# Kernel tuning notes

Hardware: AMD Instinct MI355X
Metric: run time of the kernel (lower is better)

The kernel has to match this reference:

```python
import jax, jax.numpy as jnp
import numpy as np

DECAY = 0.99
EPS = 1e-05


def setup_inputs() -> dict:
    key = jax.random.key(0)
    k1, k2 = jax.random.split(key)
    B, C, H, W = 16, 64, 32, 32
    K = 8192
    z_e = jax.random.normal(k1, (B, C, H, W), dtype=jnp.float32)
    embedding = jax.random.normal(k2, (K, C), dtype=jnp.float32)
    cluster_size = jnp.zeros((K,), dtype=jnp.float32)
    embedding_avg = embedding  # initialized as a clone of the codebook
    return {"z_e": z_e, "embedding": embedding, "cluster_size": cluster_size,
            "embedding_avg": embedding_avg}


def reference(z_e, embedding, cluster_size, embedding_avg):
    B, C, H, W = z_e.shape
    K = embedding.shape[0]
    # [N, C] tokens
    z_flat = jnp.transpose(z_e, (0, 2, 3, 1)).reshape(-1, C)
    d = ((z_flat * z_flat).sum(-1, keepdims=True)
         - 2.0 * (z_flat @ embedding.T)
         + (embedding * embedding).sum(-1))
    indices = jnp.argmin(d, axis=1)  # [N] int
    z_q_flat = embedding[indices]    # [N, C]
    z_q = jnp.transpose(z_q_flat.reshape(B, H, W, C), (0, 3, 1, 2))
    # EMA codebook update (training path); one-hot matmuls expressed as segment sums
    counts = jax.ops.segment_sum(jnp.ones(z_flat.shape[0], dtype=z_flat.dtype),
                                 indices, num_segments=K)            # encodings.sum(0)
    dw = jax.ops.segment_sum(z_flat, indices, num_segments=K)        # encodings.T @ z_flat
    new_cluster_size = DECAY * cluster_size + (1.0 - DECAY) * counts
    new_embedding_avg = DECAY * embedding_avg + (1.0 - DECAY) * dw
    n = new_cluster_size.sum()
    cs = (new_cluster_size + EPS) / (n + K * EPS) * n
    new_embedding = new_embedding_avg / cs[:, None]
    # straight-through estimator
    z_q_st = z_e + jax.lax.stop_gradient(z_q - z_e)
    return (z_q_st, indices.reshape(B, H * W), z_q,
            new_embedding, new_cluster_size, new_embedding_avg)
```

## Files before the change

kernel.cpp:

```cpp
#include <hip/hip_runtime.h>

#define DECAYF 0.99f
#define OMDF   0.01f
#define TAU    3.5e-2f

typedef unsigned int u32;
typedef unsigned long long u64;
typedef __attribute__((ext_vector_type(8))) _Float16 f16x8;
typedef __attribute__((ext_vector_type(16))) float f32x16;

#define EN_OFF     0
#define EFRAG_OFF  32768
#define IDX_OFF    32768
#define LIST_OFF   98304
#define BEST1_OFF  2129920
#define BEST2_OFF  3178496
#define CNT_OFF    3702784

__device__ __forceinline__ u64 enc_pair(float s, int idx) {
  u32 u = __float_as_uint(s);
  u = (u & 0x80000000u) ? ~u : (u | 0x80000000u);
  return ((u64)u << 32) | (u32)(~idx);
}
__device__ __forceinline__ float dec_score(u64 e) {
  u32 u = (u32)(e >> 32);
  u = (u & 0x80000000u) ? (u & 0x7fffffffu) : ~u;
  return __uint_as_float(u);
}
__device__ __forceinline__ int dec_idx(u64 e) { return (int)(~(u32)e); }
__device__ __forceinline__ unsigned short f2h(float f) {
  union { _Float16 h; unsigned short u; } v;
  v.h = (_Float16)f;
  return v.u;
}
__device__ __forceinline__ float exact_dot(const float* __restrict__ sx,
                                           const float* __restrict__ emb, int k) {
  const float4* e = (const float4*)(emb + (size_t)k * 64);
  float a = 0.f;
#pragma unroll
  for (int q = 0; q < 16; ++q) {
    float4 v = e[q];
    a = fmaf(sx[4 * q],     v.x, a);
    a = fmaf(sx[4 * q + 1], v.y, a);
    a = fmaf(sx[4 * q + 2], v.z, a);
    a = fmaf(sx[4 * q + 3], v.w, a);
  }
  return a;
}

__global__ __launch_bounds__(256) void k_prep(const float* __restrict__ emb,
                                              const float* __restrict__ cs_in,
                                              const float* __restrict__ avg_in,
                                              const float* __restrict__ z_e,
                                              float* __restrict__ en,
                                              unsigned char* __restrict__ efrag,
                                              unsigned char* __restrict__ zfrag,
                                              float* __restrict__ out4,
                                              float* __restrict__ out5,
                                              int* __restrict__ cnt,
                                              float* __restrict__ nsum) {
  __shared__ float warr[4];
  int bid = blockIdx.x;
  if (bid < 512) {
    int tid = bid * 256 + threadIdx.x;
    if (tid == 0) *cnt = 0;
    int k = tid >> 4, q = tid & 15;
    float4 v = ((const float4*)emb)[tid];
    int kstep = q >> 2, h = (q >> 1) & 1, j0 = (q & 1) * 4;
    int tile = k >> 5, n32 = k & 31;
    ushort4 hv;
    hv.x = f2h(v.x); hv.y = f2h(v.y); hv.z = f2h(v.z); hv.w = f2h(v.w);
    size_t off = (size_t)tile * 4096 + (size_t)kstep * 1024
               + (size_t)h * 512 + (size_t)n32 * 16 + (size_t)j0 * 2;
    *(ushort4*)(efrag + off) = hv;
    float s = v.x * v.x + v.y * v.y + v.z * v.z + v.w * v.w;
    s += __shfl_xor(s, 1, 16);
    s += __shfl_xor(s, 2, 16);
    s += __shfl_xor(s, 4, 16);
    s += __shfl_xor(s, 8, 16);
    if (q == 0) en[k] = 0.5f * s;
  } else if (bid < 1031) {
    int tid = (bid - 512) * 256 + threadIdx.x;
    if (tid < 131072) {
      float4 v = ((const float4*)avg_in)[tid];
      v.x *= DECAYF; v.y *= DECAYF; v.z *= DECAYF; v.w *= DECAYF;
      ((float4*)out5)[tid] = v;
    }
  } else if (bid == 1031) {
    int thr = threadIdx.x;
    float s = 0.f;
#pragma unroll
    for (int q = 0; q < 8; ++q) {
      int idx = q * 256 + thr;
      float4 v = ((const float4*)cs_in)[idx];
      v.x *= DECAYF; v.y *= DECAYF; v.z *= DECAYF; v.w *= DECAYF;
      ((float4*)out4)[idx] = v;
      s += v.x + v.y + v.z + v.w;
    }
    s += __shfl_xor(s, 1, 64);
    s += __shfl_xor(s, 2, 64);
    s += __shfl_xor(s, 4, 64);
    s += __shfl_xor(s, 8, 64);
    s += __shfl_xor(s, 16, 64);
    s += __shfl_xor(s, 32, 64);
    if ((thr & 63) == 0) warr[thr >> 6] = s;
    __syncthreads();
    if (thr == 0) *nsum = warr[0] + warr[1] + warr[2] + warr[3];
  } else {
    int t = (bid - 1032) * 256 + threadIdx.x;
    int m = t & 31, h = (t >> 5) & 1, ks = (t >> 6) & 3, tg = t >> 8;
    int token = tg * 32 + m;
    int b = token >> 10, hw = token & 1023;
    const float* zr = z_e + ((size_t)b << 16) + hw;
    int c0 = ks * 16 + h * 8;
    unsigned short u[8];
#pragma unroll
    for (int j = 0; j < 8; ++j) u[j] = f2h(zr[(size_t)(c0 + j) << 10]);
    size_t off = (size_t)tg * 4096 + (size_t)ks * 1024
               + (size_t)h * 512 + (size_t)m * 16;
    ((ushort4*)(zfrag + off))[0] = make_ushort4(u[0], u[1], u[2], u[3]);
    ((ushort4*)(zfrag + off))[1] = make_ushort4(u[4], u[5], u[6], u[7]);
  }
}

__global__ __launch_bounds__(256) void k_argmin_mfma(
    const unsigned char* __restrict__ zfrag,
    const unsigned char* __restrict__ efrag,
    const float* __restrict__ en, u64* __restrict__ best1,
    float* __restrict__ best2) {
  alignas(16) __shared__ unsigned char sbuf[2][8192];
  __shared__ float sen[1024];
  const int tb = blockIdx.x >> 3;
  const int sl = blockIdx.x & 7;
  const int wave = threadIdx.x >> 6, lane = threadIdx.x & 63;
  const int h = lane >> 5, m = lane & 31;
  const int token0 = tb * 128 + wave * 32;
  const int scb = sl << 10;

  ((float4*)sen)[threadIdx.x] = ((const float4*)(en + scb))[threadIdx.x];

  f16x8 a[4];
  {
    const unsigned char* zb = zfrag + ((size_t)(tb * 4 + wave)) * 4096
                            + (size_t)h * 512 + (size_t)m * 16;
#pragma unroll
    for (int ks = 0; ks < 4; ++ks) a[ks] = *(const f16x8*)(zb + (size_t)ks * 1024);
  }
  float b1[16], b2[16];
#pragma unroll
  for (int r = 0; r < 16; ++r) { b1[r] = -3.0e38f; b2[r] = -3.0e38f; }

  const unsigned char* gbase0 = efrag + (size_t)scb * 128;
  auto stage = [&](int ib, int buf) {
    const unsigned char* g = gbase0 + (size_t)ib * 8192 + (size_t)wave * 2048;
#pragma unroll
    for (int it = 0; it < 2; ++it) {
      __builtin_amdgcn_global_load_lds(
          (const __attribute__((address_space(1))) u32*)(g + it * 1024 + lane * 16),
          (__attribute__((address_space(3))) u32*)(&sbuf[buf][wave * 2048 + it * 1024]),
          16, 0, 0);
    }
  };
  stage(0, 0);
  for (int ib = 0; ib < 16; ++ib) {
    __syncthreads();
    if (ib < 15) stage(ib + 1, (ib + 1) & 1);
    const unsigned char* sb0 = &sbuf[ib & 1][0];
#pragma unroll
    for (int t32 = 0; t32 < 2; ++t32) {
      const int t = ib * 2 + t32;
      const float negen = -sen[t * 32 + m];
      f32x16 acc;
#pragma unroll
      for (int r = 0; r < 16; ++r) acc[r] = negen;
      const unsigned char* sb = sb0 + t32 * 4096 + h * 512 + m * 16;
#pragma unroll
      for (int ks = 0; ks < 4; ++ks) {
        f16x8 bf = *(const f16x8*)(sb + (size_t)ks * 1024);
        acc = __builtin_amdgcn_mfma_f32_32x32x16_f16(a[ks], bf, acc, 0, 0, 0);
      }
      const u32 emb6 = (u32)(63 - t);
#pragma unroll
      for (int r = 0; r < 16; ++r) {
        float f = __uint_as_float((__float_as_uint(acc[r]) & 0xFFFFFFC0u) | emb6);
        b2[r] = __builtin_amdgcn_fmed3f(f, b1[r], b2[r]);
        b1[r] = fmaxf(b1[r], f);
      }
    }
  }
  int mi[16];
#pragma unroll
  for (int r = 0; r < 16; ++r) mi[r] = m;
#pragma unroll
  for (int st = 1; st < 32; st <<= 1) {
#pragma unroll
    for (int r = 0; r < 16; ++r) {
      float ob1 = __shfl_xor(b1[r], st, 64);
      float ob2 = __shfl_xor(b2[r], st, 64);
      int omi = __shfl_xor(mi[r], st, 64);
      bool ogt = ob1 > b1[r];
      b2[r] = fmaxf(fminf(b1[r], ob1), fmaxf(b2[r], ob2));
      mi[r] = ogt ? omi : mi[r];
      b1[r] = fmaxf(b1[r], ob1);
    }
  }
  if (m == 0) {
#pragma unroll
    for (int r = 0; r < 16; ++r) {
      int row = (r & 3) + 8 * (r >> 2) + 4 * h;
      int token = token0 + row;
      int t = 63 - (int)(__float_as_uint(b1[r]) & 63u);
      int gcode = scb + t * 32 + mi[r];
      best1[(size_t)sl * 16384 + token] = enc_pair(b1[r], gcode);
      best2[(size_t)sl * 16384 + token] = b2[r];
    }
  }
}

__global__ __launch_bounds__(256) void k_resolve(const u64* __restrict__ best1,
                                                 const float* __restrict__ best2,
                                                 int* __restrict__ idxa,
                                                 int* __restrict__ list,
                                                 int* __restrict__ cnt) {
  int n = blockIdx.x * 256 + threadIdx.x;
  u64 e[8];
  float sp[8];
#pragma unroll
  for (int s = 0; s < 8; ++s) {
    e[s]  = best1[(size_t)s * 16384 + n];
    sp[s] = best2[(size_t)s * 16384 + n];
  }
  u64 top = e[0];
#pragma unroll
  for (int s = 1; s < 8; ++s) top = e[s] > top ? e[s] : top;
  float second = -3.0e38f;
#pragma unroll
  for (int s = 0; s < 8; ++s) second = fmaxf(second, sp[s]);
#pragma unroll
  for (int s = 0; s < 8; ++s)
    if (e[s] != top) second = fmaxf(second, dec_score(e[s]));
  idxa[n] = dec_idx(top);
  if (dec_score(top) - second < TAU) {
    int p = atomicAdd(cnt, 1);
    list[p] = n;
  }
}

__global__ __launch_bounds__(256) void k_fixup(const float* __restrict__ z_e,
                                               const float* __restrict__ emb,
                                               const float* __restrict__ en,
                                               const u64* __restrict__ best1,
                                               const float* __restrict__ best2,
                                               const int* __restrict__ list,
                                               const int* __restrict__ cnt,
                                               int* __restrict__ idxa) {
  __shared__ float sx[64];
  __shared__ u64 esh[8];
  __shared__ float b2sh[8];
  __shared__ int cand[8];
  __shared__ int fsl[8];
  __shared__ int ncand, nfsl;
  __shared__ u64 red;
  int count = *cnt;
  for (int i = blockIdx.x; i < count; i += gridDim.x) {
    int n = list[i];
    __syncthreads();
    if (threadIdx.x == 0) { ncand = 0; nfsl = 0; red = 0ull; }
    if (threadIdx.x < 8) {
      esh[threadIdx.x]  = best1[(size_t)threadIdx.x * 16384 + n];
      b2sh[threadIdx.x] = best2[(size_t)threadIdx.x * 16384 + n];
    }
    if (threadIdx.x < 64) {
      sx[threadIdx.x] = z_e[((size_t)(n >> 10) << 16)
                            + ((size_t)threadIdx.x << 10) + (n & 1023)];
    }
    __syncthreads();
    u64 top = esh[0];
#pragma unroll
    for (int s = 1; s < 8; ++s) top = esh[s] > top ? esh[s] : top;
    float theta = dec_score(top) - TAU;
    if (threadIdx.x < 8) {
      int s = threadIdx.x;
      if (dec_score(esh[s]) >= theta) {
        int p = atomicAdd(&ncand, 1);
        cand[p] = dec_idx(esh[s]);
      }
      if (b2sh[s] >= theta) {
        int p = atomicAdd(&nfsl, 1);
        fsl[p] = s;
      }
    }
    __syncthreads();
    u64 myb = 0ull;
    if (threadIdx.x < ncand) {
      int k = cand[threadIdx.x];
      float a = exact_dot(sx, emb, k) - en[k];
      myb = enc_pair(a, k);
    }
    int nf = nfsl;
    for (int f = 0; f < nf; ++f) {
      int s = fsl[f];
      int k0 = (s << 10) + threadIdx.x;
      float a0 = exact_dot(sx, emb, k0)       - en[k0];
      float a1 = exact_dot(sx, emb, k0 + 256) - en[k0 + 256];
      float a2 = exact_dot(sx, emb, k0 + 512) - en[k0 + 512];
      float a3 = exact_dot(sx, emb, k0 + 768) - en[k0 + 768];
      u64 m0 = enc_pair(a0, k0),       m1 = enc_pair(a1, k0 + 256);
      u64 m2 = enc_pair(a2, k0 + 512), m3 = enc_pair(a3, k0 + 768);
      u64 ma = m0 > m1 ? m0 : m1, mb = m2 > m3 ? m2 : m3;
      u64 mm = ma > mb ? ma : mb;
      myb = mm > myb ? mm : myb;
    }
    if (myb) atomicMax(&red, myb);
    __syncthreads();
    if (threadIdx.x == 0) idxa[n] = dec_idx(red);
  }
}

__global__ __launch_bounds__(256) void k_scatter(const float* __restrict__ z_e,
                                                 const int* __restrict__ idxa,
                                                 float* __restrict__ out4,
                                                 float* __restrict__ out5) {
  int tid = blockIdx.x * 256 + threadIdx.x;
  int n = tid >> 6, c = tid & 63;
  int idx = idxa[n];
  int b = n >> 10, hw = n & 1023;
  float x = z_e[((size_t)b << 16) + ((size_t)c << 10) + hw];
  atomicAdd(out5 + (size_t)idx * 64 + c, OMDF * x);
  if (c == 0) atomicAdd(out4 + idx, OMDF);
}

__global__ __launch_bounds__(256) void k_gather(const float* __restrict__ z_e,
                                                const float* __restrict__ emb,
                                                const int* __restrict__ idxa,
                                                float* __restrict__ out0,
                                                float* __restrict__ out1,
                                                float* __restrict__ out2) {
  int tid = blockIdx.x * 256 + threadIdx.x;
  int hw4 = tid & 255;
  int c   = (tid >> 8) & 63;
  int b   = tid >> 14;
  int n0  = (b << 10) + (hw4 << 2);
  size_t off = ((size_t)b << 16) + ((size_t)c << 10) + ((size_t)hw4 << 2);
  float4 z = *(const float4*)(z_e + off);
  int i0 = idxa[n0], i1 = idxa[n0 + 1], i2 = idxa[n0 + 2], i3 = idxa[n0 + 3];
  float4 q;
  q.x = emb[(size_t)i0 * 64 + c];
  q.y = emb[(size_t)i1 * 64 + c];
  q.z = emb[(size_t)i2 * 64 + c];
  q.w = emb[(size_t)i3 * 64 + c];
  float4 st;
  st.x = z.x + (q.x - z.x);
  st.y = z.y + (q.y - z.y);
  st.z = z.z + (q.z - z.z);
  st.w = z.w + (q.w - z.w);
  *(float4*)(out2 + off) = q;
  *(float4*)(out0 + off) = st;
  if (c == 0) {
    float4 f = make_float4((float)i0, (float)i1, (float)i2, (float)i3);
    *(float4*)(out1 + n0) = f;
  }
}

__global__ __launch_bounds__(256) void k_final(const float* __restrict__ out4,
                                               const float* __restrict__ out5,
                                               const float* __restrict__ nsum,
                                               float* __restrict__ out3) {
  int tid = blockIdx.x * 256 + threadIdx.x;
  int k = tid >> 4;
  double nn  = (double)*nsum + 163.84;
  double ncs = (double)out4[k];
  double cs  = (ncs + 1e-5) / (nn + 8192.0 * 1e-5) * nn;
  float inv  = (float)(1.0 / cs);
  float4 v = ((const float4*)out5)[tid];
  v.x *= inv; v.y *= inv; v.z *= inv; v.w *= inv;
  ((float4*)out3)[tid] = v;
}

extern "C" void kernel_launch(void* const* d_in, const int* in_sizes, int n_in,
                              void* d_out, int out_size, void* d_ws, size_t ws_size,
                              hipStream_t stream) {
  const float* z_e    = (const float*)d_in[0];
  const float* emb    = (const float*)d_in[1];
  const float* cs_in  = (const float*)d_in[2];
  const float* avg_in = (const float*)d_in[3];

  float* out  = (float*)d_out;
  float* out0 = out;
  float* out1 = out0 + 1048576;
  float* out2 = out1 + 16384;
  float* out3 = out2 + 1048576;
  float* out4 = out3 + 524288;
  float* out5 = out4 + 8192;

  char* ws = (char*)d_ws;
  float* en            = (float*)(ws + EN_OFF);
  unsigned char* efrag = (unsigned char*)(ws + EFRAG_OFF);
  u64* best1           = (u64*)(ws + BEST1_OFF);
  float* best2         = (float*)(ws + BEST2_OFF);
  int* idxa            = (int*)(ws + IDX_OFF);
  int* list            = (int*)(ws + LIST_OFF);
  int* cnt             = (int*)(ws + CNT_OFF);
  float* nsum          = (float*)(ws + CNT_OFF + 4);
  unsigned char* zfrag = (unsigned char*)out0;

  k_prep       <<<1544, 256, 0, stream>>>(emb, cs_in, avg_in, z_e, en, efrag,
                                          zfrag, out4, out5, cnt, nsum);
  k_argmin_mfma<<<1024, 256, 0, stream>>>(zfrag, efrag, en, best1, best2);
  k_resolve    <<<64,   256, 0, stream>>>(best1, best2, idxa, list, cnt);
  k_fixup      <<<1024, 256, 0, stream>>>(z_e, emb, en, best1, best2, list, cnt, idxa);
  k_scatter    <<<4096, 256, 0, stream>>>(z_e, idxa, out4, out5);
  k_gather     <<<1024, 256, 0, stream>>>(z_e, emb, idxa, out0, out1, out2);
  k_final      <<<512,  256, 0, stream>>>(out4, out5, nsum, out3);
}
```

Baseline: 158.2 us.

## Switch argmin GEMM to 16x16x32 MFMA with matching fragment layouts

Replaces the 32x32x16 MFMA tiling in the distance/argmin kernel with 16x16x32 MFMAs. Each wave still covers 32 tokens, now as two 16-row sets that reuse each codebook fragment load, which halves LDS B-fragment reads per MFMA. The prep kernel writes the z and codebook fp16 fragments in the new layout. The cross-lane top-2 reduction shrinks from 5 to 4 shuffle stages over 8 instead of 16 registers, cutting epilogue cost. The risk is different MFMA latency and issue behaviour, and a finer 16-code tile granularity in the packed index bits.

```diff
diff --git a/kernel.cpp b/kernel.cpp
--- a/kernel.cpp
+++ b/kernel.cpp
@@ -7,7 +7,7 @@
 typedef unsigned int u32;
 typedef unsigned long long u64;
 typedef __attribute__((ext_vector_type(8))) _Float16 f16x8;
-typedef __attribute__((ext_vector_type(16))) float f32x16;
+typedef __attribute__((ext_vector_type(4))) float f32x4;
 
 #define EN_OFF     0
 #define EFRAG_OFF  32768
@@ -66,12 +66,11 @@
     if (tid == 0) *cnt = 0;
     int k = tid >> 4, q = tid & 15;
     float4 v = ((const float4*)emb)[tid];
-    int kstep = q >> 2, h = (q >> 1) & 1, j0 = (q & 1) * 4;
-    int tile = k >> 5, n32 = k & 31;
     ushort4 hv;
     hv.x = f2h(v.x); hv.y = f2h(v.y); hv.z = f2h(v.z); hv.w = f2h(v.w);
-    size_t off = (size_t)tile * 4096 + (size_t)kstep * 1024
-               + (size_t)h * 512 + (size_t)n32 * 16 + (size_t)j0 * 2;
+    size_t off = (size_t)(k >> 4) * 2048 + (size_t)(q >> 3) * 1024
+               + (size_t)((q >> 1) & 3) * 256 + (size_t)(k & 15) * 16
+               + (size_t)(q & 1) * 8;
     *(ushort4*)(efrag + off) = hv;
     float s = v.x * v.x + v.y * v.y + v.z * v.z + v.w * v.w;
     s += __shfl_xor(s, 1, 16);
@@ -107,19 +106,17 @@
     __syncthreads();
     if (thr == 0) *nsum = warr[0] + warr[1] + warr[2] + warr[3];
   } else {
-    int t = (bid - 1032) * 256 + threadIdx.x;
-    int m = t & 31, h = (t >> 5) & 1, ks = (t >> 6) & 3, tg = t >> 8;
-    int token = tg * 32 + m;
-    int b = token >> 10, hw = token & 1023;
-    const float* zr = z_e + ((size_t)b << 16) + hw;
-    int c0 = ks * 16 + h * 8;
+    int id = (bid - 1032) * 256 + threadIdx.x;
+    int n = id & 16383, k = id >> 14;
+    int b = n >> 10, hw = n & 1023;
+    const float* zr = z_e + ((size_t)b << 16) + ((size_t)(k * 8) << 10) + hw;
     unsigned short u[8];
 #pragma unroll
-    for (int j = 0; j < 8; ++j) u[j] = f2h(zr[(size_t)(c0 + j) << 10]);
-    size_t off = (size_t)tg * 4096 + (size_t)ks * 1024
-               + (size_t)h * 512 + (size_t)m * 16;
-    ((ushort4*)(zfrag + off))[0] = make_ushort4(u[0], u[1], u[2], u[3]);
-    ((ushort4*)(zfrag + off))[1] = make_ushort4(u[4], u[5], u[6], u[7]);
+    for (int j = 0; j < 8; ++j) u[j] = f2h(zr[(size_t)j << 10]);
+    size_t off = (size_t)(n >> 4) * 2048 + (size_t)(k >> 2) * 1024
+               + (size_t)(k & 3) * 256 + (size_t)(n & 15) * 16;
+    *(ushort4*)(zfrag + off)     = make_ushort4(u[0], u[1], u[2], u[3]);
+    *(ushort4*)(zfrag + off + 8) = make_ushort4(u[4], u[5], u[6], u[7]);
   }
 }
 
@@ -133,22 +130,24 @@
   const int tb = blockIdx.x >> 3;
   const int sl = blockIdx.x & 7;
   const int wave = threadIdx.x >> 6, lane = threadIdx.x & 63;
-  const int h = lane >> 5, m = lane & 31;
+  const int col = lane & 15, g4 = lane >> 4;
   const int token0 = tb * 128 + wave * 32;
   const int scb = sl << 10;
 
   ((float4*)sen)[threadIdx.x] = ((const float4*)(en + scb))[threadIdx.x];
 
-  f16x8 a[4];
+  f16x8 a[2][2];
   {
-    const unsigned char* zb = zfrag + ((size_t)(tb * 4 + wave)) * 4096
-                            + (size_t)h * 512 + (size_t)m * 16;
-#pragma unroll
-    for (int ks = 0; ks < 4; ++ks) a[ks] = *(const f16x8*)(zb + (size_t)ks * 1024);
-  }
-  float b1[16], b2[16];
-#pragma unroll
-  for (int r = 0; r < 16; ++r) { b1[r] = -3.0e38f; b2[r] = -3.0e38f; }
+    const unsigned char* zb = zfrag + ((size_t)(tb * 8 + wave * 2)) * 2048
+                            + (size_t)g4 * 256 + (size_t)col * 16;
+    a[0][0] = *(const f16x8*)(zb);
+    a[0][1] = *(const f16x8*)(zb + 1024);
+    a[1][0] = *(const f16x8*)(zb + 2048);
+    a[1][1] = *(const f16x8*)(zb + 3072);
+  }
+  float b1[8], b2[8];
+#pragma unroll
+  for (int r = 0; r < 8; ++r) { b1[r] = -3.0e38f; b2[r] = -3.0e38f; }
 
   const unsigned char* gbase0 = efrag + (size_t)scb * 128;
   auto stage = [&](int ib, int buf) {
@@ -167,34 +166,37 @@
     if (ib < 15) stage(ib + 1, (ib + 1) & 1);
     const unsigned char* sb0 = &sbuf[ib & 1][0];
 #pragma unroll
-    for (int t32 = 0; t32 < 2; ++t32) {
-      const int t = ib * 2 + t32;
-      const float negen = -sen[t * 32 + m];
-      f32x16 acc;
-#pragma unroll
-      for (int r = 0; r < 16; ++r) acc[r] = negen;
-      const unsigned char* sb = sb0 + t32 * 4096 + h * 512 + m * 16;
-#pragma unroll
-      for (int ks = 0; ks < 4; ++ks) {
-        f16x8 bf = *(const f16x8*)(sb + (size_t)ks * 1024);
-        acc = __builtin_amdgcn_mfma_f32_32x32x16_f16(a[ks], bf, acc, 0, 0, 0);
+    for (int ct = 0; ct < 4; ++ct) {
+      const int t = ib * 4 + ct;
+      const float negen = -sen[t * 16 + col];
+      f16x8 bf0 = *(const f16x8*)(sb0 + ct * 2048 + lane * 16);
+      f16x8 bf1 = *(const f16x8*)(sb0 + ct * 2048 + 1024 + lane * 16);
+      f32x4 acc0, acc1;
+#pragma unroll
+      for (int r = 0; r < 4; ++r) { acc0[r] = negen; acc1[r] = negen; }
+      acc0 = __builtin_amdgcn_mfma_f32_16x16x32_f16(a[0][0], bf0, acc0, 0, 0, 0);
+      acc0 = __builtin_amdgcn_mfma_f32_16x16x32_f16(a[0][1], bf1, acc0, 0, 0, 0);
+      acc1 = __builtin_amdgcn_mfma_f32_16x16x32_f16(a[1][0], bf0, acc1, 0, 0, 0);
+      acc1 = __builtin_amdgcn_mfma_f32_16x16x32_f16(a[1][1], bf1, acc1, 0, 0, 0);
+      const u32 emb6 = (u32)(63 - t);
+#pragma unroll
+      for (int r = 0; r < 4; ++r) {
+        float f0 = __uint_as_float((__float_as_uint(acc0[r]) & 0xFFFFFFC0u) | emb6);
+        b2[r] = __builtin_amdgcn_fmed3f(f0, b1[r], b2[r]);
+        b1[r] = fmaxf(b1[r], f0);
+        float f1 = __uint_as_float((__float_as_uint(acc1[r]) & 0xFFFFFFC0u) | emb6);
+        b2[4 + r] = __builtin_amdgcn_fmed3f(f1, b1[4 + r], b2[4 + r]);
+        b1[4 + r] = fmaxf(b1[4 + r], f1);
       }
-      const u32 emb6 = (u32)(63 - t);
-#pragma unroll
-      for (int r = 0; r < 16; ++r) {
-        float f = __uint_as_float((__float_as_uint(acc[r]) & 0xFFFFFFC0u) | emb6);
-        b2[r] = __builtin_amdgcn_fmed3f(f, b1[r], b2[r]);
-        b1[r] = fmaxf(b1[r], f);
-      }
-    }
-  }
-  int mi[16];
-#pragma unroll
-  for (int r = 0; r < 16; ++r) mi[r] = m;
-#pragma unroll
-  for (int st = 1; st < 32; st <<= 1) {
-#pragma unroll
-    for (int r = 0; r < 16; ++r) {
+    }
+  }
+  int mi[8];
+#pragma unroll
+  for (int r = 0; r < 8; ++r) mi[r] = col;
+#pragma unroll
+  for (int st = 1; st < 16; st <<= 1) {
+#pragma unroll
+    for (int r = 0; r < 8; ++r) {
       float ob1 = __shfl_xor(b1[r], st, 64);
       float ob2 = __shfl_xor(b2[r], st, 64);
       int omi = __shfl_xor(mi[r], st, 64);
@@ -204,13 +206,13 @@
       b1[r] = fmaxf(b1[r], ob1);
     }
   }
-  if (m == 0) {
-#pragma unroll
-    for (int r = 0; r < 16; ++r) {
-      int row = (r & 3) + 8 * (r >> 2) + 4 * h;
-      int token = token0 + row;
+  if (col == 0) {
+#pragma unroll
+    for (int r = 0; r < 8; ++r) {
+      int tset = r >> 2, rr = r & 3;
+      int token = token0 + tset * 16 + g4 * 4 + rr;
       int t = 63 - (int)(__float_as_uint(b1[r]) & 63u);
-      int gcode = scb + t * 32 + mi[r];
+      int gcode = scb + t * 16 + mi[r];
       best1[(size_t)sl * 16384 + token] = enc_pair(b1[r], gcode);
       best2[(size_t)sl * 16384 + token] = b2[r];
     }
```

Result: faster. 148.9 us (-5.9%).
